# Performance work log

Hardware: AMD Instinct MI355X
Metric: run time of the kernel (lower is better)

The kernel has to match this reference:

```python
import jax, jax.numpy as jnp
import numpy as np

N_ITER = 50


def sparsemax_bisect(X, n_iter=N_ITER):
    # entmax-style bisection for sparsemax (alpha=2): p = clip(X - tau, 0), sum(p) = 1
    d = X.shape[-1]
    max_val = jnp.max(X, axis=-1, keepdims=True)          # [N, 1]
    tau_lo = max_val - 1.0                                # f(tau_lo) >= 0
    tau_hi = max_val - 1.0 / d                            # f(tau_hi) <= 0
    f_lo = jnp.sum(jnp.clip(X - tau_lo, 0.0), axis=-1, keepdims=True) - 1.0
    dm0 = tau_hi - tau_lo

    def body(_, carry):
        tau_lo, dm, _tau_m = carry
        dm = dm * 0.5
        tau_m = tau_lo + dm
        f_m = jnp.sum(jnp.clip(X - tau_m, 0.0), axis=-1, keepdims=True) - 1.0
        tau_lo = jnp.where(f_m * f_lo >= 0, tau_m, tau_lo)
        return (tau_lo, dm, tau_m)

    _, _, tau_m = jax.lax.fori_loop(0, n_iter, body, (tau_lo, dm0, tau_lo))
    # p from the final midpoint, exactly as in entmax's sparsemax_bisect
    return jnp.clip(X - tau_m, 0.0)


def setup_inputs() -> dict:
    key = jax.random.key(0)
    X = jax.random.normal(key, (4096, 32000), dtype=jnp.float32)
    return {"X": X}


def reference(X):
    p_star = sparsemax_bisect(X, N_ITER)
    p_star = p_star / jnp.sum(p_star, axis=-1, keepdims=True)
    # log(0) -> -inf, matching torch.log on exact zeros
    sup = p_star > 0
    return jnp.where(sup, jnp.log(jnp.where(sup, p_star, 1.0)), -jnp.inf)
```

## Files before the change

### kernel.cpp

```cpp
#include <hip/hip_runtime.h>
#include <math.h>


typedef float f32x4 __attribute__((ext_vector_type(4)));

#define ROWS 4096
#define COLS 32000
#define NV4  (COLS / 4)
#define TPB  256
#define WPB  (TPB / 64)
#define U    8
#define SEG  512
#define CAP  (SEG * WPB)
#define REGC 4
#define QMIN (1e-37f)

__global__ __launch_bounds__(TPB, 8)
void logsparsemax_v6_kernel(const float* __restrict__ X,
                            float* __restrict__ Y) {
    __shared__ float s_cand[CAP];
    __shared__ int   s_cidx[CAP];
    __shared__ float s_wmax[WPB];
    __shared__ int   s_wcnt[WPB];
    __shared__ float s_res[2];

    const float SENT = __uint_as_float(0xDEDEDEDEu);

    const int tid  = threadIdx.x;
    const int lane = tid & 63;
    const int wid  = tid >> 6;
    const int row  = blockIdx.x;
    const float* __restrict__ Xr = X + (size_t)row * COLS;
    const f32x4* __restrict__ X4 = (const f32x4*)Xr;
    float* __restrict__ Yr = Y + (size_t)row * COLS;

    const int sbase = wid * SEG;
    float wmax = -INFINITY;
    float thr  = INFINITY;
    int   cnt  = 0;

    thr = -INFINITY;

    int i = tid;
    for (; i + (U - 1) * TPB < NV4; i += U * TPB) {
        f32x4 v[U];
        #pragma unroll
        for (int u = 0; u < U; ++u) v[u] = X4[i + u * TPB];

        float mall = -INFINITY;
        #pragma unroll
        for (int u = 0; u < U; ++u)
            mall = fmaxf(mall, fmaxf(fmaxf(v[u].x, v[u].y), fmaxf(v[u].z, v[u].w)));

        if (__ballot(mall > thr) != 0ull) {
            float t = mall;
            #pragma unroll
            for (int off = 32; off > 0; off >>= 1)
                t = fmaxf(t, __shfl_xor(t, off, 64));
            wmax = fmaxf(wmax, t);
            thr  = wmax - 1.0f;
            #pragma unroll
            for (int u = 0; u < U; ++u) {
                #pragma unroll
                for (int c = 0; c < 4; ++c) {
                    float val = (c == 0) ? v[u].x : (c == 1) ? v[u].y : (c == 2) ? v[u].z : v[u].w;
                    bool p = val > thr;
                    unsigned long long m = __ballot(p);
                    if (m != 0ull) {
                        if (p) {
                            int pos = cnt + __popcll(m & ((1ull << lane) - 1ull));
                            if (pos < SEG) {
                                s_cand[sbase + pos] = val;
                                s_cidx[sbase + pos] = 4 * (i + u * TPB) + c;
                            }
                        }
                        cnt += __popcll(m);
                    }
                }
            }
        }
    }
    for (; i < NV4; i += TPB) {
        f32x4 a = X4[i];
        float mall = fmaxf(fmaxf(a.x, a.y), fmaxf(a.z, a.w));
        if (__ballot(mall > thr) != 0ull) {
            float t = mall;
            #pragma unroll
            for (int off = 32; off > 0; off >>= 1)
                t = fmaxf(t, __shfl_xor(t, off, 64));
            wmax = fmaxf(wmax, t);
            thr  = wmax - 1.0f;
            float vv[4] = {a.x, a.y, a.z, a.w};
            #pragma unroll
            for (int c = 0; c < 4; ++c) {
                bool p = vv[c] > thr;
                unsigned long long m = __ballot(p);
                if (m != 0ull) {
                    if (p) {
                        int pos = cnt + __popcll(m & ((1ull << lane) - 1ull));
                        if (pos < SEG) {
                            s_cand[sbase + pos] = vv[c];
                            s_cidx[sbase + pos] = 4 * i + c;
                        }
                    }
                    cnt += __popcll(m);
                }
            }
        }
    }

    if (lane == 0) { s_wmax[wid] = wmax; s_wcnt[wid] = cnt; }
    __syncthreads();

    const float bmax = fmaxf(fmaxf(s_wmax[0], s_wmax[1]), fmaxf(s_wmax[2], s_wmax[3]));
    const float tau_lo0 = bmax - 1.0f;
    const float tau_hi0 = bmax - (float)(1.0 / (double)COLS);
    const bool  fast = (s_wcnt[0] <= SEG) && (s_wcnt[1] <= SEG) &&
                       (s_wcnt[2] <= SEG) && (s_wcnt[3] <= SEG);

    if (wid == 0) {
        int nf = 0;
        if (fast) {
            for (int w = 0; w < WPB; ++w) {
                const int cw = s_wcnt[w];
                for (int j0 = 0; j0 < cw; j0 += 64) {
                    const int j = j0 + lane;
                    const bool in = (j < cw);
                    float v  = in ? s_cand[w * SEG + j] : 0.0f;
                    int   ix = in ? s_cidx[w * SEG + j] : 0;
                    bool  k  = in && (v > tau_lo0);
                    unsigned long long m = __ballot(k);
                    if (k) {
                        int pos = nf + __popcll(m & ((1ull << lane) - 1ull));
                        s_cand[pos] = v;
                        s_cidx[pos] = ix;
                    }
                    nf += __popcll(m);
                }
            }
        }

        float creg[REGC];
        #pragma unroll
        for (int k = 0; k < REGC; ++k) {
            int j = lane + 64 * k;
            creg[k] = (fast && j < nf) ? s_cand[j] : SENT;
        }

        auto fsum = [&](float tau) -> float {
            float acc = 0.0f;
            if (fast) {
                #pragma unroll
                for (int k = 0; k < REGC; ++k) acc += fmaxf(creg[k] - tau, 0.0f);
                for (int j = 64 * REGC + lane; j < nf; j += 64)
                    acc += fmaxf(s_cand[j] - tau, 0.0f);
            } else {
                for (int j = lane; j < COLS; j += 64)
                    acc += fmaxf(Xr[j] - tau, 0.0f);
            }
            #pragma unroll
            for (int off = 32; off > 0; off >>= 1)
                acc += __shfl_xor(acc, off, 64);
            return acc;
        };

        float tau_lo = tau_lo0;
        float dm     = tau_hi0 - tau_lo0;
        float tau_m  = tau_lo;
        const float f_lo = fsum(tau_lo) - 1.0f;
        for (int it = 0; it < 50; ++it) {
            dm *= 0.5f;
            float tcur = tau_lo + dm;
            tau_m = tcur;
            if (tcur == tau_lo) break;
            float f_m = fsum(tcur) - 1.0f;
            if (f_m * f_lo >= 0.0f) tau_lo = tcur;
        }
        const float ssum = fsum(tau_m);
        if (lane == 0) { s_res[0] = tau_m; s_res[1] = ssum; }

        if (fast) {
            const float lsm = logf(fmaxf(ssum, QMIN));
            for (int j = lane; j < nf; j += 64) {
                float r = s_cand[j] - tau_m;
                if (r > 0.0f)
                    Yr[s_cidx[j]] = logf(fmaxf(r, QMIN)) - lsm;
            }
        }
    }
    __syncthreads();

    if (!fast) {
        const float tau = s_res[0];
        const float lsm = logf(fmaxf(s_res[1], QMIN));
        f32x4* __restrict__ Y4 = (f32x4*)Yr;
        for (int v4i = tid; v4i < NV4; v4i += TPB) {
            f32x4 v = X4[v4i];
            f32x4 o;
            float r;
            r = v.x - tau; o.x = (r > 0.0f) ? logf(fmaxf(r, QMIN)) - lsm : SENT;
            r = v.y - tau; o.y = (r > 0.0f) ? logf(fmaxf(r, QMIN)) - lsm : SENT;
            r = v.z - tau; o.z = (r > 0.0f) ? logf(fmaxf(r, QMIN)) - lsm : SENT;
            r = v.w - tau; o.w = (r > 0.0f) ? logf(fmaxf(r, QMIN)) - lsm : SENT;
            Y4[v4i] = o;
        }
    }
}

extern "C" void kernel_launch(void* const* d_in, const int* in_sizes, int n_in,
                              void* d_out, int out_size, void* d_ws, size_t ws_size,
                              hipStream_t stream) {
    const float* X = (const float*)d_in[0];
    float* Y = (float*)d_out;
    hipMemsetAsync(d_out, 0xDE, (size_t)out_size * sizeof(float), stream);
    logsparsemax_v6_kernel<<<dim3(ROWS), dim3(TPB), 0, stream>>>(X, Y);
}
```

Measured before the change: 238.4 us.

## Fuse output sentinel fill into scan and software-pipeline row loads

Drops the separate hipMemsetAsync and has the scan loop write the sentinel value to each output vector as it reads the input. This fuses the fill into the single pass and removes a separate launch and full write pass. The scan loop is now double-buffered: the next group of loads is issued before the current one is processed, with the unroll reduced from 8 to 4 and the launch bound relaxed to 6 blocks. The sentinel changes from the 0xDE byte pattern to -1e38, and the fast-path scatter writes must still land after the fill, which the same threads handle in program order.

After: 221.7 us. 1.08x faster.

```diff
diff --git a/kernel.cpp b/kernel.cpp
--- a/kernel.cpp
+++ b/kernel.cpp
@@ -9,22 +9,21 @@
 #define NV4  (COLS / 4)
 #define TPB  256
 #define WPB  (TPB / 64)
-#define U    8
+#define U    4
 #define SEG  512
 #define CAP  (SEG * WPB)
 #define REGC 4
+#define SENT (-1e38f)
 #define QMIN (1e-37f)
 
-__global__ __launch_bounds__(TPB, 8)
-void logsparsemax_v6_kernel(const float* __restrict__ X,
+__global__ __launch_bounds__(TPB, 6)
+void logsparsemax_v8_kernel(const float* __restrict__ X,
                             float* __restrict__ Y) {
     __shared__ float s_cand[CAP];
     __shared__ int   s_cidx[CAP];
     __shared__ float s_wmax[WPB];
     __shared__ int   s_wcnt[WPB];
     __shared__ float s_res[2];
-
-    const float SENT = __uint_as_float(0xDEDEDEDEu);
 
     const int tid  = threadIdx.x;
     const int lane = tid & 63;
@@ -33,24 +32,35 @@
     const float* __restrict__ Xr = X + (size_t)row * COLS;
     const f32x4* __restrict__ X4 = (const f32x4*)Xr;
     float* __restrict__ Yr = Y + (size_t)row * COLS;
-
+    f32x4* __restrict__ Y4 = (f32x4*)Yr;
+
+    const f32x4 sent4 = {SENT, SENT, SENT, SENT};
     const int sbase = wid * SEG;
+
     float wmax = -INFINITY;
-    float thr  = INFINITY;
+    float thr  = -INFINITY;
     int   cnt  = 0;
 
-    thr = -INFINITY;
-
     int i = tid;
-    for (; i + (U - 1) * TPB < NV4; i += U * TPB) {
-        f32x4 v[U];
-        #pragma unroll
-        for (int u = 0; u < U; ++u) v[u] = X4[i + u * TPB];
+    f32x4 cur[U];
+    #pragma unroll
+    for (int u = 0; u < U; ++u) cur[u] = X4[i + u * TPB];
+
+    while (i + (U - 1) * TPB < NV4) {
+        const int inext = i + U * TPB;
+        const bool hn = (inext + (U - 1) * TPB < NV4);
+        f32x4 nxt[U];
+        if (hn) {
+            #pragma unroll
+            for (int u = 0; u < U; ++u) nxt[u] = X4[inext + u * TPB];
+        }
+        #pragma unroll
+        for (int u = 0; u < U; ++u) Y4[i + u * TPB] = sent4;
 
         float mall = -INFINITY;
         #pragma unroll
         for (int u = 0; u < U; ++u)
-            mall = fmaxf(mall, fmaxf(fmaxf(v[u].x, v[u].y), fmaxf(v[u].z, v[u].w)));
+            mall = fmaxf(mall, fmaxf(fmaxf(cur[u].x, cur[u].y), fmaxf(cur[u].z, cur[u].w)));
 
         if (__ballot(mall > thr) != 0ull) {
             float t = mall;
@@ -61,27 +71,30 @@
             thr  = wmax - 1.0f;
             #pragma unroll
             for (int u = 0; u < U; ++u) {
+                float vv[4] = {cur[u].x, cur[u].y, cur[u].z, cur[u].w};
                 #pragma unroll
                 for (int c = 0; c < 4; ++c) {
-                    float val = (c == 0) ? v[u].x : (c == 1) ? v[u].y : (c == 2) ? v[u].z : v[u].w;
-                    bool p = val > thr;
+                    bool p = vv[c] > thr;
                     unsigned long long m = __ballot(p);
-                    if (m != 0ull) {
-                        if (p) {
-                            int pos = cnt + __popcll(m & ((1ull << lane) - 1ull));
-                            if (pos < SEG) {
-                                s_cand[sbase + pos] = val;
-                                s_cidx[sbase + pos] = 4 * (i + u * TPB) + c;
-                            }
+                    if (p) {
+                        int pos = cnt + __popcll(m & ((1ull << lane) - 1ull));
+                        if (pos < SEG) {
+                            s_cand[sbase + pos] = vv[c];
+                            s_cidx[sbase + pos] = 4 * (i + u * TPB) + c;
                         }
-                        cnt += __popcll(m);
                     }
+                    cnt += __popcll(m);
                 }
             }
         }
+
+        #pragma unroll
+        for (int u = 0; u < U; ++u) cur[u] = nxt[u];
+        i = inext;
     }
     for (; i < NV4; i += TPB) {
         f32x4 a = X4[i];
+        Y4[i] = sent4;
         float mall = fmaxf(fmaxf(a.x, a.y), fmaxf(a.z, a.w));
         if (__ballot(mall > thr) != 0ull) {
             float t = mall;
@@ -95,16 +108,14 @@
             for (int c = 0; c < 4; ++c) {
                 bool p = vv[c] > thr;
                 unsigned long long m = __ballot(p);
-                if (m != 0ull) {
-                    if (p) {
-                        int pos = cnt + __popcll(m & ((1ull << lane) - 1ull));
-                        if (pos < SEG) {
-                            s_cand[sbase + pos] = vv[c];
-                            s_cidx[sbase + pos] = 4 * i + c;
-                        }
+                if (p) {
+                    int pos = cnt + __popcll(m & ((1ull << lane) - 1ull));
+                    if (pos < SEG) {
+                        s_cand[sbase + pos] = vv[c];
+                        s_cidx[sbase + pos] = 4 * i + c;
                     }
-                    cnt += __popcll(m);
                 }
+                cnt += __popcll(m);
             }
         }
     }
@@ -193,7 +204,6 @@
     if (!fast) {
         const float tau = s_res[0];
         const float lsm = logf(fmaxf(s_res[1], QMIN));
-        f32x4* __restrict__ Y4 = (f32x4*)Yr;
         for (int v4i = tid; v4i < NV4; v4i += TPB) {
             f32x4 v = X4[v4i];
             f32x4 o;
@@ -212,6 +222,5 @@
                               hipStream_t stream) {
     const float* X = (const float*)d_in[0];
     float* Y = (float*)d_out;
-    hipMemsetAsync(d_out, 0xDE, (size_t)out_size * sizeof(float), stream);
-    logsparsemax_v6_kernel<<<dim3(ROWS), dim3(TPB), 0, stream>>>(X, Y);
+    logsparsemax_v8_kernel<<<dim3(ROWS), dim3(TPB), 0, stream>>>(X, Y);
 }
```
